# Kernel tuning notes

Measured on AMD Instinct MI355X. Metric: run time of the kernel, lower is better.

Reference implementation:

```python
import jax, jax.numpy as jnp
import numpy as np

B, N, V, T = 16, 1024, 4096, 8


def _lsa(cost):
    """Jonker-Volgenant linear sum assignment on a square [n,n] cost matrix.
    Returns (row_ind, col_ind) minimizing cost[row, col].sum(). Equivalent to
    scipy.optimize.linear_sum_assignment for square matrices."""
    n = cost.shape[0]
    INF = np.inf
    u = np.zeros(n + 1)
    v = np.zeros(n + 1)
    p = np.zeros(n + 1, dtype=np.int64)    # p[j] = row assigned to column j (1-based)
    way = np.zeros(n + 1, dtype=np.int64)
    for i in range(1, n + 1):
        p[0] = i
        j0 = 0
        minv = np.full(n + 1, INF)
        used = np.zeros(n + 1, dtype=bool)
        while True:
            used[j0] = True
            i0 = p[j0]
            free = ~used
            free[0] = False
            cur = cost[i0 - 1, :] - u[i0] - v[1:]
            upd = free[1:] & (cur < minv[1:])
            minv[1:][upd] = cur[upd]
            way[1:][upd] = j0
            j1 = int(np.argmin(np.where(free[1:], minv[1:], INF))) + 1
            delta = minv[j1]
            u[p[used]] += delta
            v[used] -= delta
            minv[~used] -= delta
            j0 = j1
            if p[j0] == 0:
                break
        while j0:
            j1 = way[j0]
            p[j0] = p[j1]
            j0 = j1
    col_of_row = np.empty(n, dtype=np.int64)
    for j in range(1, n + 1):
        col_of_row[p[j] - 1] = j - 1
    return np.arange(n), col_of_row


def _compute_assignment(lp_np, gt_np, types_np, mask_np):
    """For each (sample, node_type) group of masked nodes, Hungarian-match
    positions to gt tokens. Returns flat (batch_idx, pos_idx, tok_idx) of all
    matched pairs. Mirrors the original type-wise padded loop (k==1 is identity)."""
    Bn = lp_np.shape[0]
    b_l, p_l, t_l = [], [], []
    for t in np.unique(types_np):
        for b in range(Bn):
            idx = np.nonzero((types_np[b] == t) & mask_np[b])[0]
            k = idx.size
            if k == 0:
                continue
            g = gt_np[b, idx]
            if k == 1:
                r = np.zeros(1, dtype=np.int64)
                c = np.zeros(1, dtype=np.int64)
            else:
                cost = -lp_np[b, idx][:, g]  # [k, k]
                r, c = _lsa(cost)
            b_l.append(np.full(k, b, dtype=np.int64))
            p_l.append(idx[r])
            t_l.append(g[c])
    return np.concatenate(b_l), np.concatenate(p_l), np.concatenate(t_l)


def setup_inputs() -> dict:
    key = jax.random.key(0)
    k1, k2, k3, k4 = jax.random.split(key, 4)
    logits = jax.random.normal(k1, (B, N, V), dtype=jnp.float32)
    gt_tokens = jax.random.randint(k2, (B, N), 0, V)
    node_types = jax.random.randint(k3, (B, N), 0, T)
    mask_positions = jax.random.randint(k4, (B, N), 0, 2).astype(bool)
    return {"logits": logits, "gt_tokens": gt_tokens,
            "node_types": node_types, "mask_positions": mask_positions}


def reference(logits, gt_tokens, node_types, mask_positions):
    # Dense log-softmax over vocab (the memory-bound bulk of the op).
    log_probs = jax.nn.log_softmax(logits, axis=-1)
    # Assignment is computed on detached values (matches .detach() in original).
    b_idx, p_idx, t_idx = _compute_assignment(
        np.asarray(jax.lax.stop_gradient(log_probs)),
        np.asarray(gt_tokens), np.asarray(node_types), np.asarray(mask_positions))
    total = b_idx.shape[0]  # total matched (masked) tokens
    sel = log_probs[jnp.asarray(b_idx), jnp.asarray(p_idx), jnp.asarray(t_idx)]
    # avg_loss = sum_b(loss_per_sample*count)/total_count == sum of matched NLL / total
    return -sel.sum() / jnp.asarray(total, sel.dtype)
```

## Files before the change

kernel.cpp:

```cpp
#include <hip/hip_runtime.h>
#include <math.h>

#define BB 16
#define NN 1024
#define VV 4096
#define TT 8
#define NG (BB*TT)
#define KMAX 124
#define STRIDE 124

__device__ __forceinline__ float wave_sum(float v){
  #pragma unroll
  for (int off = 32; off; off >>= 1) v += __shfl_down(v, off);
  return v;
}

__device__ __forceinline__ unsigned fkey(float f){
  unsigned b = __float_as_uint(f);
  return b ^ ((unsigned)((int)b >> 31) | 0x80000000u);
}
__device__ __forceinline__ float inv_fkey(unsigned u){
  unsigned b = (u & 0x80000000u) ? (u ^ 0x80000000u) : ~u;
  return __uint_as_float(b);
}

__device__ __forceinline__ unsigned dpp_min64(unsigned x){
  unsigned t;
  t = (unsigned)__builtin_amdgcn_update_dpp(-1, (int)x, 0x111, 0xF, 0xF, false); x = x < t ? x : t;
  t = (unsigned)__builtin_amdgcn_update_dpp(-1, (int)x, 0x112, 0xF, 0xF, false); x = x < t ? x : t;
  t = (unsigned)__builtin_amdgcn_update_dpp(-1, (int)x, 0x114, 0xF, 0xF, false); x = x < t ? x : t;
  t = (unsigned)__builtin_amdgcn_update_dpp(-1, (int)x, 0x118, 0xF, 0xF, false); x = x < t ? x : t;
  t = (unsigned)__builtin_amdgcn_update_dpp(-1, (int)x, 0x142, 0xF, 0xF, false); x = x < t ? x : t;
  t = (unsigned)__builtin_amdgcn_update_dpp(-1, (int)x, 0x143, 0xF, 0xF, false); x = x < t ? x : t;
  return x;
}

__global__ __launch_bounds__(64) void k_main(const float* __restrict__ logits,
                                             const int* __restrict__ types,
                                             const int* __restrict__ gt,
                                             const unsigned char* __restrict__ raw,
                                             int* __restrict__ kcnt,
                                             float* __restrict__ gval,
                                             float* __restrict__ lse){
  int lane = threadIdx.x;

  if (blockIdx.x >= NG){
    int row = blockIdx.x - NG;
    uchar4 pv = ((const uchar4*)raw)[lane];
    bool bool_layout = (__ballot((pv.y | pv.z | pv.w) != 0) != 0ull);
    int mv = bool_layout ? (int)raw[row] : ((const int*)raw)[row];
    if (mv == 0){ if (lane == 0) lse[row] = 0.f; return; }

    const float4* x = (const float4*)(logits + (size_t)row * VV);
    float4 v[16];
    #pragma unroll
    for (int i = 0; i < 16; i++) v[i] = x[lane + 64*i];
    float m = -INFINITY;
    #pragma unroll
    for (int i = 0; i < 16; i++)
      m = fmaxf(m, fmaxf(fmaxf(v[i].x, v[i].y), fmaxf(v[i].z, v[i].w)));
    #pragma unroll
    for (int off = 32; off; off >>= 1) m = fmaxf(m, __shfl_xor(m, off));
    float s = 0.f;
    #pragma unroll
    for (int i = 0; i < 16; i++)
      s += __expf(v[i].x - m) + __expf(v[i].y - m)
         + __expf(v[i].z - m) + __expf(v[i].w - m);
    #pragma unroll
    for (int off = 32; off; off >>= 1) s += __shfl_xor(s, off);
    if (lane == 0) lse[row] = m + __logf(s);
    return;
  }

  __shared__ float Cm[KMAX*STRIDE];
  __shared__ float u_l[KMAX+1];
  __shared__ int   p_l[KMAX+1];
  __shared__ int   way_l[KMAX+1];
  __shared__ int   rowown[KMAX];
  __shared__ int   listA[KMAX];
  __shared__ int   listB[KMAX];
  int g = blockIdx.x, b = g >> 3, t = g & 7;
  unsigned long long lm = (1ull << lane) - 1ull;

  int local = 0;
  const uchar4* r4 = (const uchar4*)raw;
  #pragma unroll
  for (int r = 0; r < 4; r++){ uchar4 u = r4[lane + 64*r]; local |= (u.y | u.z | u.w); }
  bool bool_layout = (__ballot(local != 0) != 0ull);
  const int* rawi = (const int*)raw;
  int base = 0;
  for (int r = 0; r < NN/64; r++){
    int pos = r*64 + lane, o = b*NN + pos;
    int mv = bool_layout ? (int)raw[o] : rawi[o];
    bool pred = (types[o] == t) && (mv != 0);
    unsigned long long ball = __ballot(pred);
    int dst = base + __popcll(ball & lm);
    if (pred && dst < KMAX){ way_l[dst] = pos; listA[dst] = gt[o]; }
    base += __popcll(ball);
  }
  int k = (base > KMAX) ? KMAX : base;
  if (lane == 0) kcnt[g] = k;
  if (k == 0){ if (lane == 0) gval[g] = 0.f; return; }

  int col0 = lane + 1, col1 = lane + 65;
  bool a0 = (col0 <= k), a1 = (col1 <= k);
  int gc0 = a0 ? listA[lane]      : 0;
  int gc1 = a1 ? listA[lane + 64] : 0;

  u_l[col0] = 0.f; p_l[col0] = 0;
  if (col1 <= KMAX){ u_l[col1] = 0.f; p_l[col1] = 0; }
  if (lane == 0){ u_l[0] = 0.f; p_l[0] = 0; }
  rowown[lane] = -1;
  if (lane + 64 < KMAX) rowown[lane+64] = -1;
  __syncthreads();

  const size_t rowbase = (size_t)b * NN;
  for (int i = 0; i < k; i += 8){
    float xs0[8], xs1[8]; int rr[8];
    #pragma unroll
    for (int s = 0; s < 8; s++){
      int r = i + s; r = (r < k) ? r : (k - 1); rr[s] = r;
      const float* q = logits + (rowbase + way_l[r]) * VV;
      xs0[s] = q[gc0]; xs1[s] = q[gc1];
    }
    #pragma unroll
    for (int s = 0; s < 8; s++){
      Cm[rr[s]*STRIDE + lane]      = -xs0[s];
      Cm[rr[s]*STRIDE + 64 + lane] = -xs1[s];
    }
  }
  __syncthreads();

  float v0 = 0.f, v1 = 0.f;
  int ra0 = -1, ra1 = -1;
  if (a0){ float m = INFINITY; int rm = 0;
    for (int i = 0; i < k; i++){ float c = Cm[i*STRIDE + lane]; if (c < m){ m = c; rm = i; } }
    v0 = m; ra0 = rm; }
  if (a1){ float m = INFINITY; int rm = 0;
    for (int i = 0; i < k; i++){ float c = Cm[i*STRIDE + 64 + lane]; if (c < m){ m = c; rm = i; } }
    v1 = m; ra1 = rm; }
  if (a0){ if (atomicCAS(&rowown[ra0], -1, col0) == -1) p_l[col0] = ra0 + 1; }
  if (a1){ if (atomicCAS(&rowown[ra1], -1, col1) == -1) p_l[col1] = ra1 + 1; }
  __syncthreads();

  bool f0 = (lane < k)    && (rowown[lane]    == -1);
  bool f1 = (lane+64 < k) && (rowown[lane+64] == -1);
  unsigned long long B0 = __ballot(f0), B1 = __ballot(f1);
  int n0 = __popcll(B0);
  if (f0) listA[__popcll(B0 & lm)]      = lane + 1;
  if (f1) listA[n0 + __popcll(B1 & lm)] = lane + 65;
  int nCur = n0 + __popcll(B1);
  __syncthreads();

  int* curL = listA; int* nxtL = listB;
  for (int pass = 0; pass < 3; pass++){
    int nNxt = 0;
    for (int fr = 0; fr < nCur; fr++){
      int row = curL[fr];
      int off = (row - 1) * STRIDE;
      float rc0 = a0 ? (Cm[off + lane]      - v0) : INFINITY;
      float rc1 = a1 ? (Cm[off + 64 + lane] - v1) : INFINITY;
      unsigned k0 = fkey(rc0), k1 = fkey(rc1);
      unsigned kk = k0 < k1 ? k0 : k1;
      unsigned m1 = (unsigned)__builtin_amdgcn_readlane((int)dpp_min64(kk), 63);
      int cand = (k0 == m1) ? col0 : ((k1 == m1) ? col1 : 0);
      unsigned long long bl1 = __ballot(cand != 0);
      int ow1 = __ffsll(bl1) - 1;
      int j1 = __builtin_amdgcn_readlane(cand, ow1);
      float u1 = inv_fkey(m1);
      unsigned k0b = (col0 == j1) ? 0xFFFFFFFFu : k0;
      unsigned k1b = (col1 == j1) ? 0xFFFFFFFFu : k1;
      unsigned kkb = k0b < k1b ? k0b : k1b;
      unsigned m2 = (unsigned)__builtin_amdgcn_readlane((int)dpp_min64(kkb), 63);
      float u2 = inv_fkey(m2);
      int jt = j1;
      if (u1 < u2){
        if (col0 == j1) v0 -= (u2 - u1);
        if (col1 == j1) v1 -= (u2 - u1);
      } else {
        int own1 = p_l[j1];
        if (own1 != 0){
          int cand2 = (k0b == m2) ? col0 : ((k1b == m2) ? col1 : 0);
          unsigned long long bl2 = __ballot(cand2 != 0);
          int ow2 = __ffsll(bl2) - 1;
          jt = __builtin_amdgcn_readlane(cand2, ow2);
        }
      }
      int iprev = p_l[jt];
      if (lane == 0){ p_l[jt] = row; u_l[row] = u2; }
      if (iprev != 0){ if (lane == 0) nxtL[nNxt] = iprev; nNxt++; }
      __syncthreads();
    }
    int* tmp = curL; curL = nxtL; nxtL = tmp;
    nCur = nNxt;
  }

  for (int fr = 0; fr < nCur; fr++){
    int irow = curL[fr];
    int rp0 = a0 ? p_l[col0] : 0;
    int rp1 = a1 ? p_l[col1] : 0;
    float rpu0 = (rp0 > 0) ? u_l[rp0] : 0.f;
    float rpu1 = (rp1 > 0) ? u_l[rp1] : 0.f;
    int off = (irow - 1) * STRIDE;
    float dist0 = a0 ? (Cm[off + lane]      - v0) : INFINITY;
    float dist1 = a1 ? (Cm[off + 64 + lane] - v1) : INFINITY;
    int way0 = 0, way1 = 0;
    bool used0 = false, used1 = false;
    int j_end; float delta_end;
    while (true){
      unsigned q0 = (a0 && !used0) ? ((fkey(dist0) & 0xFFFFFF80u) | (unsigned)(col0-1)) : 0xFFFFFFFFu;
      unsigned q1 = (a1 && !used1) ? ((fkey(dist1) & 0xFFFFFF80u) | (unsigned)(col1-1)) : 0xFFFFFFFFu;
      unsigned key = q0 < q1 ? q0 : q1;
      unsigned kmin = (unsigned)__builtin_amdgcn_readlane((int)dpp_min64(key), 63);
      int j1 = (int)(kmin & 127u) + 1;
      int owner = (j1-1) & 63, slot = (j1-1) >> 6;
      float dsel  = slot ? dist1 : dist0;
      int   psel  = slot ? rp1   : rp0;
      float pusel = slot ? rpu1  : rpu0;
      float delta = __uint_as_float((unsigned)__builtin_amdgcn_readlane(__float_as_int(dsel), owner));
      int   i0    = __builtin_amdgcn_readlane(psel, owner);
      float pu    = __uint_as_float((unsigned)__builtin_amdgcn_readlane(__float_as_int(pusel), owner));
      used0 |= (j1 == col0);
      used1 |= (j1 == col1);
      if (i0 == 0){ j_end = j1; delta_end = delta; break; }
      float bse = delta - pu;
      int o2 = (i0 - 1) * STRIDE;
      float c0 = Cm[o2 + lane];
      float c1 = Cm[o2 + 64 + lane];
      float nd0 = bse + c0 - v0;
      float nd1 = bse + c1 - v1;
      if (a0 && !used0 && (nd0 < dist0)){ dist0 = nd0; way0 = j1; }
      if (a1 && !used1 && (nd1 < dist1)){ dist1 = nd1; way1 = j1; }
    }
    if (used0){ float adj = delta_end - dist0; v0 -= adj; u_l[rp0] = rpu0 + adj; }
    if (used1){ float adj = delta_end - dist1; v1 -= adj; u_l[rp1] = rpu1 + adj; }
    if (lane == 0) u_l[irow] = delta_end;
    if (a0) way_l[col0] = way0;
    if (a1) way_l[col1] = way1;
    __syncthreads();
    int j0 = j_end;
    while (true){
      int jw = way_l[j0];
      int pr = p_l[jw];
      int pw = (jw == 0) ? irow : pr;
      if (lane == 0) p_l[j0] = pw;
      if (jw == 0) break;
      j0 = jw;
    }
    __syncthreads();
  }

  __syncthreads();
  float acc = 0.f;
  if (a0) acc += Cm[(p_l[col0]-1)*STRIDE + lane];
  if (a1) acc += Cm[(p_l[col1]-1)*STRIDE + 64 + lane];
  acc = wave_sum(acc);
  if (lane == 0) gval[g] = -acc;
}

__global__ __launch_bounds__(256) void k_final(const float* __restrict__ lse,
                                               const int* __restrict__ kcnt,
                                               const float* __restrict__ gval,
                                               float* __restrict__ out){
  __shared__ double sd[256];
  __shared__ double sg[256];
  __shared__ int    si[256];
  int tid = threadIdx.x;
  double s = 0.0, gs = 0.0; int c = 0;
  for (int i = tid; i < BB*NN; i += 256) s += (double)lse[i];
  for (int i = tid; i < NG; i += 256){ gs += (double)gval[i]; c += kcnt[i]; }
  sd[tid] = s; sg[tid] = gs; si[tid] = c;
  __syncthreads();
  for (int off = 128; off; off >>= 1){
    if (tid < off){ sd[tid] += sd[tid+off]; sg[tid] += sg[tid+off]; si[tid] += si[tid+off]; }
    __syncthreads();
  }
  if (tid == 0) out[0] = (float)((sd[0] - sg[0]) / (double)si[0]);
}

extern "C" void kernel_launch(void* const* d_in, const int* in_sizes, int n_in,
                              void* d_out, int out_size, void* d_ws, size_t ws_size,
                              hipStream_t stream) {
  const float* logits = (const float*)d_in[0];
  const int*   gt     = (const int*)d_in[1];
  const int*   types  = (const int*)d_in[2];
  const unsigned char* maskraw = (const unsigned char*)d_in[3];
  float* out = (float*)d_out;

  char* w = (char*)d_ws;
  float* lse  = (float*)w;  w += (size_t)BB*NN*4;
  int*   kcnt = (int*)w;    w += 1024;
  float* gval = (float*)w;  w += 1024;

  k_main <<<NG + BB*NN, 64, 0, stream>>>(logits, types, gt, maskraw, kcnt, gval, lse);
  k_final<<<1, 256, 0, stream>>>(lse, kcnt, gval, out);
}
```

Before: 431.4 us.

## Process eight rows per LSE block with double-buffered register loads

Each log-sum-exp block now handles eight consecutive rows instead of one, which cuts the block count by eight. Within a block, the next masked row's logits are loaded into a second register buffer while the current row is reduced, so memory latency overlaps with compute. Register pressure rises (two 16-float4 buffers), which may lower occupancy. Masked-out rows are still skipped and get zero written.

```diff
diff --git a/kernel.cpp b/kernel.cpp
--- a/kernel.cpp
+++ b/kernel.cpp
@@ -8,6 +8,7 @@
 #define NG (BB*TT)
 #define KMAX 124
 #define STRIDE 124
+#define LSEROWS 8
 
 __device__ __forceinline__ float wave_sum(float v){
   #pragma unroll
@@ -35,6 +36,28 @@
   return x;
 }
 
+__device__ __forceinline__ void lse_load(const float4* __restrict__ x, int lane,
+                                         float4 (&v)[16]){
+  #pragma unroll
+  for (int i = 0; i < 16; i++) v[i] = x[lane + 64*i];
+}
+__device__ __forceinline__ float lse_reduce(const float4 (&v)[16]){
+  float m = -INFINITY;
+  #pragma unroll
+  for (int i = 0; i < 16; i++)
+    m = fmaxf(m, fmaxf(fmaxf(v[i].x, v[i].y), fmaxf(v[i].z, v[i].w)));
+  #pragma unroll
+  for (int off = 32; off; off >>= 1) m = fmaxf(m, __shfl_xor(m, off));
+  float s = 0.f;
+  #pragma unroll
+  for (int i = 0; i < 16; i++)
+    s += __expf(v[i].x - m) + __expf(v[i].y - m)
+       + __expf(v[i].z - m) + __expf(v[i].w - m);
+  #pragma unroll
+  for (int off = 32; off; off >>= 1) s += __shfl_xor(s, off);
+  return m + __logf(s);
+}
+
 __global__ __launch_bounds__(64) void k_main(const float* __restrict__ logits,
                                              const int* __restrict__ types,
                                              const int* __restrict__ gt,
@@ -45,30 +68,46 @@
   int lane = threadIdx.x;
 
   if (blockIdx.x >= NG){
-    int row = blockIdx.x - NG;
+    int rbase = (blockIdx.x - NG) * LSEROWS;
     uchar4 pv = ((const uchar4*)raw)[lane];
     bool bool_layout = (__ballot((pv.y | pv.z | pv.w) != 0) != 0ull);
-    int mv = bool_layout ? (int)raw[row] : ((const int*)raw)[row];
-    if (mv == 0){ if (lane == 0) lse[row] = 0.f; return; }
-
-    const float4* x = (const float4*)(logits + (size_t)row * VV);
-    float4 v[16];
+    const int* rawi = (const int*)raw;
+    unsigned mb = 0;
     #pragma unroll
-    for (int i = 0; i < 16; i++) v[i] = x[lane + 64*i];
-    float m = -INFINITY;
-    #pragma unroll
-    for (int i = 0; i < 16; i++)
-      m = fmaxf(m, fmaxf(fmaxf(v[i].x, v[i].y), fmaxf(v[i].z, v[i].w)));
-    #pragma unroll
-    for (int off = 32; off; off >>= 1) m = fmaxf(m, __shfl_xor(m, off));
-    float s = 0.f;
-    #pragma unroll
-    for (int i = 0; i < 16; i++)
-      s += __expf(v[i].x - m) + __expf(v[i].y - m)
-         + __expf(v[i].z - m) + __expf(v[i].w - m);
-    #pragma unroll
-    for (int off = 32; off; off >>= 1) s += __shfl_xor(s, off);
-    if (lane == 0) lse[row] = m + __logf(s);
+    for (int r = 0; r < LSEROWS; r++){
+      int mv = bool_layout ? (int)raw[rbase + r] : rawi[rbase + r];
+      mb |= (mv != 0) ? (1u << r) : 0u;
+    }
+    if (lane == 0){
+      #pragma unroll
+      for (int r = 0; r < LSEROWS; r++)
+        if (!(mb & (1u << r))) lse[rbase + r] = 0.f;
+    }
+    if (mb == 0) return;
+
+    float4 A[16], Bf[16];
+    int rA = __ffs(mb) - 1;
+    unsigned rem = mb & ~(1u << rA);
+    lse_load((const float4*)(logits + (size_t)(rbase + rA) * VV), lane, A);
+    while (true){
+      int rB = rem ? (__ffs(rem) - 1) : -1;
+      if (rB >= 0){
+        rem &= ~(1u << rB);
+        lse_load((const float4*)(logits + (size_t)(rbase + rB) * VV), lane, Bf);
+      }
+      float la = lse_reduce(A);
+      if (lane == 0) lse[rbase + rA] = la;
+      if (rB < 0) break;
+      int rC = rem ? (__ffs(rem) - 1) : -1;
+      if (rC >= 0){
+        rem &= ~(1u << rC);
+        lse_load((const float4*)(logits + (size_t)(rbase + rC) * VV), lane, A);
+      }
+      float lb = lse_reduce(Bf);
+      if (lane == 0) lse[rbase + rB] = lb;
+      if (rC < 0) break;
+      rA = rC;
+    }
     return;
   }
 
@@ -292,6 +331,6 @@
   int*   kcnt = (int*)w;    w += 1024;
   float* gval = (float*)w;  w += 1024;
 
-  k_main <<<NG + BB*NN, 64, 0, stream>>>(logits, types, gt, maskraw, kcnt, gval, lse);
+  k_main <<<NG + (BB*NN)/LSEROWS, 64, 0, stream>>>(logits, types, gt, maskraw, kcnt, gval, lse);
   k_final<<<1, 256, 0, stream>>>(lse, kcnt, gval, out);
 }
```

Measured after the change: 434.3 us. No clear change (+0.7%).
